# Kernel optimization log

Measured on AMD Instinct MI355X. Metric: run time of the kernel, lower is better.

Reference implementation:

```python
import jax, jax.numpy as jnp
import numpy as np

# Decode-stage paged attention with ALiBi (HPU flat-PA style):
# batch2block scatter of queries, per-block QK + alibi bias, segment-wise
# stable softmax over each sequence's blocks, AV matmul, block2batch reduce.
BATCH = 32          # decode sequences
H = 32              # query heads
KVH = 8             # kv heads (GQA)
QPK = H // KVH      # queries per kv head
D = 128             # head size
BS = 128            # block size (tokens per KV-cache block)
BLOCKS_PER_SEQ = 16 # context 2048 tokens per sequence
U = BATCH * BLOCKS_PER_SEQ  # 512 used blocks
NB = 600            # total blocks in cache pool
SCALE = 1.0 / float(np.sqrt(D))
NEG = -1e30


def setup_inputs() -> dict:
    key = jax.random.key(0)
    k0, k1, k2 = jax.random.split(key, 3)
    query = jax.random.normal(k0, (BATCH, H, D), jnp.float32)
    key_cache = jax.random.normal(k1, (NB, BS, KVH, D), jnp.float32)
    value_cache = jax.random.normal(k2, (NB, BS, KVH, D), jnp.float32)
    # contiguous PA: used blocks are the first U blocks of the pool
    block_list = jnp.arange(U, dtype=jnp.int32)
    # each sequence owns BLOCKS_PER_SEQ consecutive blocks
    block_groups = (jnp.arange(U, dtype=jnp.int32) // BLOCKS_PER_SEQ).astype(jnp.int32)
    # all blocks fully used (context = BLOCKS_PER_SEQ*BS exactly)
    block_usage = jnp.full((U,), BS, dtype=jnp.int32)
    # alibi_blocks[u, p] = (global position) - (context_len - 1)  (<= 0)
    ctx = BLOCKS_PER_SEQ * BS
    pos = (jnp.arange(U) % BLOCKS_PER_SEQ)[:, None] * BS + jnp.arange(BS)[None, :]
    alibi_blocks = (pos - (ctx - 1)).astype(jnp.float32)
    # standard geometric alibi slopes: 2^(-8*(i+1)/H)
    alibi_slopes = 2.0 ** (-(jnp.arange(1, H + 1, dtype=jnp.float32)) * (8.0 / H))
    return dict(query=query, key_cache=key_cache, value_cache=value_cache,
                alibi_blocks=alibi_blocks, alibi_slopes=alibi_slopes,
                block_list=block_list, block_groups=block_groups,
                block_usage=block_usage)


def reference(query, key_cache, value_cache, alibi_blocks, alibi_slopes,
              block_list, block_groups, block_usage):
    # gather KV blocks from the paged cache
    K = key_cache[block_list]            # [U, BS, KVH, D]
    V = value_cache[block_list]          # [U, BS, KVH, D]
    # batch2block: replicate each sequence's query onto its blocks
    q = query[block_groups] * SCALE      # [U, H, D]
    qg = q.reshape(U, KVH, QPK, D)
    # QK^T per block (GQA: each kv head serves QPK query heads)
    scores = jnp.einsum('ugqd,ukgd->ugqk', qg, K).reshape(U, H, BS)
    # decode alibi bias: [U, H, BS] = alibi_blocks[:,None,:] * slopes[None,:,None]
    scores = scores + alibi_blocks[:, None, :] * alibi_slopes[None, :, None]
    # mask unused slots within each block
    valid = jnp.arange(BS, dtype=jnp.int32)[None, :] < block_usage[:, None]  # [U, BS]
    scores = jnp.where(valid[:, None, :], scores, NEG)
    # stable softmax across all blocks of each sequence (segment-wise)
    bmax = scores.max(-1)                                            # [U, H]
    gmax = jax.ops.segment_max(bmax, block_groups, num_segments=BATCH)
    e = jnp.exp(scores - gmax[block_groups][:, :, None])             # [U, H, BS]
    e = jnp.where(valid[:, None, :], e, 0.0)
    bsum = e.sum(-1)                                                 # [U, H]
    gsum = jax.ops.segment_sum(bsum, block_groups, num_segments=BATCH)  # [B, H]
    # AV per block, then block2batch reduce
    eg = e.reshape(U, KVH, QPK, BS)
    av = jnp.einsum('ugqk,ukgd->ugqd', eg, V).reshape(U, H, D)       # [U, H, D]
    out = jax.ops.segment_sum(av, block_groups, num_segments=BATCH)  # [B, H, D]
    out = out / gsum[:, :, None]
    return out.reshape(BATCH, H * D)
```

## Files before the change

### kernel.cpp

```cpp
#include <hip/hip_runtime.h>
#include <stdint.h>

#define BATCH 32
#define NH    32
#define KVH   8
#define QPK   4
#define DH    128
#define BS    128
#define NEG   (-1e30f)
#define SCALEF 0.08838834764831845f
#define MAXU  64
#define NSP   4
#define CHK   16
#define KVROW (KVH * DH)

#define GAS __attribute__((address_space(1)))
#define LAS __attribute__((address_space(3)))

__global__ __launch_bounds__(128, 2)
void pa_partial(const float* __restrict__ query,
                const float* __restrict__ key_cache,
                const float* __restrict__ value_cache,
                const float* __restrict__ alibi_blocks,
                const float* __restrict__ alibi_slopes,
                const int* __restrict__ block_list,
                const int* __restrict__ block_groups,
                const int* __restrict__ block_usage,
                float* __restrict__ Mp, float* __restrict__ Sp,
                float* __restrict__ Op, int U) {
  __shared__ __align__(16) float Kbuf[2][2][CHK * DH];
  __shared__ __align__(16) float q_lds[QPK * DH];
  __shared__ __align__(16) float p_lds[2][CHK * QPK];
  __shared__ float combO[2][QPK][DH];
  __shared__ float combM[2][QPK];
  __shared__ float combS[2][QPK];
  __shared__ int ulist[MAXU], pblds[MAXU], uslds[MAXU];
  __shared__ int ucount;

  const int tid  = threadIdx.x;
  const int w    = tid >> 6;
  const int lane = tid & 63;
  const int r32  = lane & 31;
  const int half = lane >> 5;
  const int r16  = lane & 15;
  const int dq   = lane >> 4;
  const int bid  = blockIdx.x;
  const int b    = bid >> 5;
  const int g    = (bid >> 2) & 7;
  const int s    = bid & 3;
  const int T0   = s * 32 + w * CHK;

  if (w == 0) {
    int cnt = 0;
    for (int base = 0; base < U; base += 64) {
      const int u = base + lane;
      const bool match = (u < U) && (block_groups[u] == b);
      const unsigned long long mk = __ballot(match);
      if (match) {
        const int pre = __popcll(mk & ((1ull << lane) - 1ull));
        if (cnt + pre < MAXU) ulist[cnt + pre] = u;
      }
      cnt += __popcll(mk);
    }
    if (cnt > MAXU) cnt = MAXU;
    if (lane == 0) ucount = cnt;
    for (int i = lane; i < cnt; i += 64) {
      const int u = ulist[i];
      pblds[i] = block_list[u];
      uslds[i] = block_usage[u];
    }
  }

  {
    const float* qsrc = query + ((size_t)b * NH + g * QPK) * DH;
    for (int e = tid; e < QPK * DH; e += 128) q_lds[e] = qsrc[e] * SCALEF;
  }

  float slope[QPK];
#pragma unroll
  for (int qh = 0; qh < QPK; ++qh) slope[qh] = alibi_slopes[g * QPK + qh];

  __syncthreads();

  const int nblk = ucount;

  float m[QPK], sacc[QPK], O[QPK][4];
#pragma unroll
  for (int qh = 0; qh < QPK; ++qh) {
    m[qh] = NEG; sacc[qh] = 0.f;
#pragma unroll
    for (int k = 0; k < 4; ++k) O[qh][k] = 0.f;
  }

  int cur = 0;
  int u_c = 0, pb_c = 0, us_c = 0;
  if (nblk > 0) {
    u_c = ulist[0]; pb_c = pblds[0]; us_c = uslds[0];
    const float* kbase = key_cache + ((size_t)pb_c * BS + T0) * KVROW + g * DH;
    float* dst = &Kbuf[w][0][0];
#pragma unroll
    for (int seg = 0; seg < 8; ++seg) {
      const int t  = 2 * seg + half;
      const int sg = r32 ^ t;
      __builtin_amdgcn_global_load_lds((const GAS void*)(kbase + (size_t)t * KVROW + sg * 4),
                                       (LAS void*)(dst + seg * 256), 16, 0, 0);
    }
  }

  for (int c = 0; c < nblk; ++c) {
    __builtin_amdgcn_sched_barrier(0);
    asm volatile("s_waitcnt vmcnt(0)" ::: "memory");
    __builtin_amdgcn_sched_barrier(0);

    const float ab = alibi_blocks[(size_t)u_c * BS + T0 + r16];
    const bool has_nxt = (c + 1 < nblk);
    int u_n = 0, pb_n = 0, us_n = 0;
    if (has_nxt) { u_n = ulist[c + 1]; pb_n = pblds[c + 1]; us_n = uslds[c + 1]; }

    const float* vb = value_cache + ((size_t)pb_c * BS + T0 + half) * KVROW
                    + g * DH + r32 * 4;
    float4 vreg[8];
#pragma unroll
    for (int tp = 0; tp < 8; ++tp)
      vreg[tp] = *(const float4*)&vb[(size_t)tp * 2 * KVROW];

    __builtin_amdgcn_sched_barrier(0);
    if (has_nxt) {
      const float* kbase = key_cache + ((size_t)pb_n * BS + T0) * KVROW + g * DH;
      float* dst = &Kbuf[w][cur ^ 1][0];
#pragma unroll
      for (int seg = 0; seg < 8; ++seg) {
        const int t  = 2 * seg + half;
        const int sg = r32 ^ t;
        __builtin_amdgcn_global_load_lds((const GAS void*)(kbase + (size_t)t * KVROW + sg * 4),
                                         (LAS void*)(dst + seg * 256), 16, 0, 0);
      }
    }
    __builtin_amdgcn_sched_barrier(0);

    const float* kb = &Kbuf[w][cur][0];
    float acc[QPK] = {0.f, 0.f, 0.f, 0.f};
#pragma unroll
    for (int i = 0; i < 8; ++i) {
      const int pos = (dq * 8 + i) ^ r16;
      const float4 kv = *(const float4*)&kb[r16 * DH + pos * 4];
      const int qo = (dq * 8 + i) * 4;
#pragma unroll
      for (int qh = 0; qh < QPK; ++qh) {
        const float4 qv = *(const float4*)&q_lds[qh * DH + qo];
        acc[qh] += kv.x * qv.x + kv.y * qv.y + kv.z * qv.z + kv.w * qv.w;
      }
    }

    const bool valid = (T0 + r16) < us_c;
    float p[QPK];
#pragma unroll
    for (int qh = 0; qh < QPK; ++qh) {
      float sc = acc[qh] + __shfl_xor(acc[qh], 16);
      sc += __shfl_xor(sc, 32);
      sc += ab * slope[qh];
      if (!valid) sc = NEG;
      float cm = sc;
#pragma unroll
      for (int off = 1; off < 16; off <<= 1) cm = fmaxf(cm, __shfl_xor(cm, off));
      const float mnew = fmaxf(m[qh], cm);
      const float rs   = __expf(m[qh] - mnew);
      m[qh] = mnew;
      p[qh] = valid ? __expf(sc - mnew) : 0.f;
      sacc[qh] = sacc[qh] * rs + ((lane < 16) ? p[qh] : 0.f);
#pragma unroll
      for (int k = 0; k < 4; ++k) O[qh][k] *= rs;
    }
    if (lane < 16)
      *(float4*)&p_lds[w][r16 * 4] = make_float4(p[0], p[1], p[2], p[3]);

#pragma unroll
    for (int tp = 0; tp < 8; ++tp) {
      const float4 pv = *(const float4*)&p_lds[w][(2 * tp + half) * 4];
      const float4 vv = vreg[tp];
      O[0][0]+=pv.x*vv.x; O[0][1]+=pv.x*vv.y; O[0][2]+=pv.x*vv.z; O[0][3]+=pv.x*vv.w;
      O[1][0]+=pv.y*vv.x; O[1][1]+=pv.y*vv.y; O[1][2]+=pv.y*vv.z; O[1][3]+=pv.y*vv.w;
      O[2][0]+=pv.z*vv.x; O[2][1]+=pv.z*vv.y; O[2][2]+=pv.z*vv.z; O[2][3]+=pv.z*vv.w;
      O[3][0]+=pv.w*vv.x; O[3][1]+=pv.w*vv.y; O[3][2]+=pv.w*vv.z; O[3][3]+=pv.w*vv.w;
    }

    u_c = u_n; pb_c = pb_n; us_c = us_n;
    cur ^= 1;
  }

#pragma unroll
  for (int qh = 0; qh < QPK; ++qh) {
    float sv = sacc[qh];
#pragma unroll
    for (int off = 1; off < 64; off <<= 1) sv += __shfl_xor(sv, off);
#pragma unroll
    for (int k = 0; k < 4; ++k) O[qh][k] += __shfl_xor(O[qh][k], 32);
    if (half == 0) {
#pragma unroll
      for (int k = 0; k < 4; ++k) combO[w][qh][r32 * 4 + k] = O[qh][k];
    }
    if (lane == 0) { combM[w][qh] = m[qh]; combS[w][qh] = sv; }
  }
  __syncthreads();

  for (int e = tid; e < QPK * DH; e += 128) {
    const int qh = e >> 7, d = e & 127;
    const float M  = fmaxf(combM[0][qh], combM[1][qh]);
    const float f0 = __expf(combM[0][qh] - M);
    const float f1 = __expf(combM[1][qh] - M);
    const float S  = f0 * combS[0][qh] + f1 * combS[1][qh];
    const float Ov = f0 * combO[0][qh][d] + f1 * combO[1][qh][d];
    const int P = ((b * KVH + g) * QPK + qh) * NSP + s;
    Op[(size_t)P * DH + d] = Ov;
    if (d == 0) { Mp[P] = M; Sp[P] = S; }
  }
}

__global__ __launch_bounds__(256, 1)
void pa_combine(const float* __restrict__ Mp, const float* __restrict__ Sp,
                const float* __restrict__ Op, float* __restrict__ out) {
  const int e  = blockIdx.x * 256 + threadIdx.x;
  const int d  = e & 127;
  const int h  = (e >> 7) & 31;
  const int bb = e >> 12;
  const int gg = h >> 2, qh = h & 3;
  const int P  = ((bb * KVH + gg) * QPK + qh) * NSP;
  float M = NEG;
#pragma unroll
  for (int sp = 0; sp < NSP; ++sp) M = fmaxf(M, Mp[P + sp]);
  float S = 0.f, Ov = 0.f;
#pragma unroll
  for (int sp = 0; sp < NSP; ++sp) {
    const float f = __expf(Mp[P + sp] - M);
    S  += f * Sp[P + sp];
    Ov += f * Op[(size_t)(P + sp) * DH + d];
  }
  out[e] = Ov / S;
}

extern "C" void kernel_launch(void* const* d_in, const int* in_sizes, int n_in,
                              void* d_out, int out_size, void* d_ws, size_t ws_size,
                              hipStream_t stream) {
  (void)n_in; (void)out_size; (void)ws_size;
  const float* query        = (const float*)d_in[0];
  const float* key_cache    = (const float*)d_in[1];
  const float* value_cache  = (const float*)d_in[2];
  const float* alibi_blocks = (const float*)d_in[3];
  const float* alibi_slopes = (const float*)d_in[4];
  const int*   block_list   = (const int*)d_in[5];
  const int*   block_groups = (const int*)d_in[6];
  const int*   block_usage  = (const int*)d_in[7];
  float*       out          = (float*)d_out;
  const int U = in_sizes[5];

  const int NP = BATCH * KVH * QPK * NSP;
  float* Mp = (float*)d_ws;
  float* Sp = Mp + NP;
  float* Op = Sp + NP;

  pa_partial<<<dim3(BATCH * KVH * NSP), dim3(128), 0, stream>>>(
      query, key_cache, value_cache, alibi_blocks, alibi_slopes,
      block_list, block_groups, block_usage, Mp, Sp, Op, U);

  pa_combine<<<dim3(BATCH * NH * DH / 256), dim3(256), 0, stream>>>(Mp, Sp, Op, out);
}
```

Baseline: 109.2 us.

## Double-buffer V registers and prefetch next block, pad Q LDS, reuse Kbuf for combine

```diff
diff --git a/kernel.cpp b/kernel.cpp
--- a/kernel.cpp
+++ b/kernel.cpp
@@ -29,11 +29,8 @@
                 float* __restrict__ Mp, float* __restrict__ Sp,
                 float* __restrict__ Op, int U) {
   __shared__ __align__(16) float Kbuf[2][2][CHK * DH];
-  __shared__ __align__(16) float q_lds[QPK * DH];
+  __shared__ __align__(16) float q_lds[QPK * 4 * 9 * 4];
   __shared__ __align__(16) float p_lds[2][CHK * QPK];
-  __shared__ float combO[2][QPK][DH];
-  __shared__ float combM[2][QPK];
-  __shared__ float combS[2][QPK];
   __shared__ int ulist[MAXU], pblds[MAXU], uslds[MAXU];
   __shared__ int ucount;
 
@@ -73,7 +70,11 @@
 
   {
     const float* qsrc = query + ((size_t)b * NH + g * QPK) * DH;
-    for (int e = tid; e < QPK * DH; e += 128) q_lds[e] = qsrc[e] * SCALEF;
+    for (int e = tid; e < QPK * DH; e += 128) {
+      const int qh = e >> 7, idx = e & 127;
+      const int qq = idx >> 5, ii = (idx >> 2) & 7, kk = idx & 3;
+      q_lds[((qh * 4 + qq) * 9 + ii) * 4 + kk] = qsrc[e] * SCALEF;
+    }
   }
 
   float slope[QPK];
@@ -94,40 +95,14 @@
 
   int cur = 0;
   int u_c = 0, pb_c = 0, us_c = 0;
+  float ab_c = 0.f;
+  float4 vA[8], vB[8];
+
   if (nblk > 0) {
     u_c = ulist[0]; pb_c = pblds[0]; us_c = uslds[0];
-    const float* kbase = key_cache + ((size_t)pb_c * BS + T0) * KVROW + g * DH;
-    float* dst = &Kbuf[w][0][0];
-#pragma unroll
-    for (int seg = 0; seg < 8; ++seg) {
-      const int t  = 2 * seg + half;
-      const int sg = r32 ^ t;
-      __builtin_amdgcn_global_load_lds((const GAS void*)(kbase + (size_t)t * KVROW + sg * 4),
-                                       (LAS void*)(dst + seg * 256), 16, 0, 0);
-    }
-  }
-
-  for (int c = 0; c < nblk; ++c) {
-    __builtin_amdgcn_sched_barrier(0);
-    asm volatile("s_waitcnt vmcnt(0)" ::: "memory");
-    __builtin_amdgcn_sched_barrier(0);
-
-    const float ab = alibi_blocks[(size_t)u_c * BS + T0 + r16];
-    const bool has_nxt = (c + 1 < nblk);
-    int u_n = 0, pb_n = 0, us_n = 0;
-    if (has_nxt) { u_n = ulist[c + 1]; pb_n = pblds[c + 1]; us_n = uslds[c + 1]; }
-
-    const float* vb = value_cache + ((size_t)pb_c * BS + T0 + half) * KVROW
-                    + g * DH + r32 * 4;
-    float4 vreg[8];
-#pragma unroll
-    for (int tp = 0; tp < 8; ++tp)
-      vreg[tp] = *(const float4*)&vb[(size_t)tp * 2 * KVROW];
-
-    __builtin_amdgcn_sched_barrier(0);
-    if (has_nxt) {
-      const float* kbase = key_cache + ((size_t)pb_n * BS + T0) * KVROW + g * DH;
-      float* dst = &Kbuf[w][cur ^ 1][0];
+    {
+      const float* kbase = key_cache + ((size_t)pb_c * BS + T0) * KVROW + g * DH;
+      float* dst = &Kbuf[w][0][0];
 #pragma unroll
       for (int seg = 0; seg < 8; ++seg) {
         const int t  = 2 * seg + half;
@@ -137,6 +112,37 @@
       }
     }
     __builtin_amdgcn_sched_barrier(0);
+    {
+      const float* vb = value_cache + ((size_t)pb_c * BS + T0 + half) * KVROW
+                      + g * DH + r32 * 4;
+#pragma unroll
+      for (int tp = 0; tp < 8; ++tp)
+        vA[tp] = *(const float4*)&vb[(size_t)tp * 2 * KVROW];
+      ab_c = alibi_blocks[(size_t)u_c * BS + T0 + r16];
+    }
+  }
+
+  for (int c = 0; c < nblk; ++c) {
+    __builtin_amdgcn_sched_barrier(0);
+    asm volatile("s_waitcnt vmcnt(5)" ::: "memory");
+    __builtin_amdgcn_sched_barrier(0);
+
+    const bool has_nxt = (c + 1 < nblk);
+    int u_n = 0, pb_n = 0, us_n = 0;
+    if (has_nxt) { u_n = ulist[c + 1]; pb_n = pblds[c + 1]; us_n = uslds[c + 1]; }
+
+    if (has_nxt) {
+      const float* kbase = key_cache + ((size_t)pb_n * BS + T0) * KVROW + g * DH;
+      float* dst = &Kbuf[w][cur ^ 1][0];
+#pragma unroll
+      for (int seg = 0; seg < 8; ++seg) {
+        const int t  = 2 * seg + half;
+        const int sg = r32 ^ t;
+        __builtin_amdgcn_global_load_lds((const GAS void*)(kbase + (size_t)t * KVROW + sg * 4),
+                                         (LAS void*)(dst + seg * 256), 16, 0, 0);
+      }
+    }
+    __builtin_amdgcn_sched_barrier(0);
 
     const float* kb = &Kbuf[w][cur][0];
     float acc[QPK] = {0.f, 0.f, 0.f, 0.f};
@@ -144,12 +150,22 @@
     for (int i = 0; i < 8; ++i) {
       const int pos = (dq * 8 + i) ^ r16;
       const float4 kv = *(const float4*)&kb[r16 * DH + pos * 4];
-      const int qo = (dq * 8 + i) * 4;
 #pragma unroll
       for (int qh = 0; qh < QPK; ++qh) {
-        const float4 qv = *(const float4*)&q_lds[qh * DH + qo];
+        const float4 qv = *(const float4*)&q_lds[((qh * 4 + dq) * 9 + i) * 4];
         acc[qh] += kv.x * qv.x + kv.y * qv.y + kv.z * qv.z + kv.w * qv.w;
       }
+    }
+
+    float4* vn = (cur == 0) ? vB : vA;
+    float ab_n = 0.f;
+    if (has_nxt) {
+      const float* vb = value_cache + ((size_t)pb_n * BS + T0 + half) * KVROW
+                      + g * DH + r32 * 4;
+#pragma unroll
+      for (int tp = 0; tp < 8; ++tp)
+        vn[tp] = *(const float4*)&vb[(size_t)tp * 2 * KVROW];
+      ab_n = alibi_blocks[(size_t)u_n * BS + T0 + r16];
     }
 
     const bool valid = (T0 + r16) < us_c;
@@ -158,7 +174,7 @@
     for (int qh = 0; qh < QPK; ++qh) {
       float sc = acc[qh] + __shfl_xor(acc[qh], 16);
       sc += __shfl_xor(sc, 32);
-      sc += ab * slope[qh];
+      sc += ab_c * slope[qh];
       if (!valid) sc = NEG;
       float cm = sc;
 #pragma unroll
@@ -174,20 +190,23 @@
     if (lane < 16)
       *(float4*)&p_lds[w][r16 * 4] = make_float4(p[0], p[1], p[2], p[3]);
 
+    const float4* vc = (cur == 0) ? vA : vB;
 #pragma unroll
     for (int tp = 0; tp < 8; ++tp) {
       const float4 pv = *(const float4*)&p_lds[w][(2 * tp + half) * 4];
-      const float4 vv = vreg[tp];
+      const float4 vv = vc[tp];
       O[0][0]+=pv.x*vv.x; O[0][1]+=pv.x*vv.y; O[0][2]+=pv.x*vv.z; O[0][3]+=pv.x*vv.w;
       O[1][0]+=pv.y*vv.x; O[1][1]+=pv.y*vv.y; O[1][2]+=pv.y*vv.z; O[1][3]+=pv.y*vv.w;
       O[2][0]+=pv.z*vv.x; O[2][1]+=pv.z*vv.y; O[2][2]+=pv.z*vv.z; O[2][3]+=pv.z*vv.w;
       O[3][0]+=pv.w*vv.x; O[3][1]+=pv.w*vv.y; O[3][2]+=pv.w*vv.z; O[3][3]+=pv.w*vv.w;
     }
 
-    u_c = u_n; pb_c = pb_n; us_c = us_n;
+    u_c = u_n; pb_c = pb_n; us_c = us_n; ab_c = ab_n;
     cur ^= 1;
   }
 
+  float* cO  = &Kbuf[w][0][0];
+  float* cMS = &Kbuf[w][1][0];
 #pragma unroll
   for (int qh = 0; qh < QPK; ++qh) {
     float sv = sacc[qh];
@@ -197,19 +216,19 @@
     for (int k = 0; k < 4; ++k) O[qh][k] += __shfl_xor(O[qh][k], 32);
     if (half == 0) {
 #pragma unroll
-      for (int k = 0; k < 4; ++k) combO[w][qh][r32 * 4 + k] = O[qh][k];
-    }
-    if (lane == 0) { combM[w][qh] = m[qh]; combS[w][qh] = sv; }
+      for (int k = 0; k < 4; ++k) cO[qh * DH + r32 * 4 + k] = O[qh][k];
+    }
+    if (lane == 0) { cMS[qh] = m[qh]; cMS[4 + qh] = sv; }
   }
   __syncthreads();
 
   for (int e = tid; e < QPK * DH; e += 128) {
     const int qh = e >> 7, d = e & 127;
-    const float M  = fmaxf(combM[0][qh], combM[1][qh]);
-    const float f0 = __expf(combM[0][qh] - M);
-    const float f1 = __expf(combM[1][qh] - M);
-    const float S  = f0 * combS[0][qh] + f1 * combS[1][qh];
-    const float Ov = f0 * combO[0][qh][d] + f1 * combO[1][qh][d];
+    const float M  = fmaxf(Kbuf[0][1][qh], Kbuf[1][1][qh]);
+    const float f0 = __expf(Kbuf[0][1][qh] - M);
+    const float f1 = __expf(Kbuf[1][1][qh] - M);
+    const float S  = f0 * Kbuf[0][1][4 + qh] + f1 * Kbuf[1][1][4 + qh];
+    const float Ov = f0 * Kbuf[0][0][qh * DH + d] + f1 * Kbuf[1][0][qh * DH + d];
     const int P = ((b * KVH + g) * QPK + qh) * NSP + s;
     Op[(size_t)P * DH + d] = Ov;
     if (d == 0) { Mp[P] = M; Sp[P] = S; }
```

Result: slower. 191.7 us (+75.5%).
